# Performance work log

Hardware: AMD Instinct MI355X
Metric: run time of the kernel (lower is better)

The kernel has to match this reference:

```python
import jax, jax.numpy as jnp
import numpy as np
from jax import lax

B = 32768
IMG = 28
K = 3
OUT_HW = IMG - K + 1  # 26
FLAT = OUT_HW * OUT_HW  # 676
HID = 300
NCLS = 10


def setup_inputs() -> dict:
    key = jax.random.key(0)
    ks = jax.random.split(key, 8)
    x = jax.random.normal(ks[0], (B, IMG * IMG), dtype=jnp.float32)
    conv_w = jax.random.normal(ks[1], (K, K), dtype=jnp.float32) * 0.1
    # Linear params stored as (in, out) so forward is h @ W + b
    W1 = jax.random.normal(ks[2], (FLAT, HID), dtype=jnp.float32) * 0.04
    b1 = jnp.zeros((HID,), dtype=jnp.float32)
    W2 = jax.random.normal(ks[3], (HID, HID), dtype=jnp.float32) * 0.06
    b2 = jnp.zeros((HID,), dtype=jnp.float32)
    W3 = jax.random.normal(ks[4], (HID, NCLS), dtype=jnp.float32) * 0.06
    b3 = jnp.zeros((NCLS,), dtype=jnp.float32)
    return {"x": x, "conv_w": conv_w, "W1": W1, "b1": b1,
            "W2": W2, "b2": b2, "W3": W3, "b3": b3}


def reference(x, conv_w, W1, b1, W2, b2, W3, b3):
    b = x.shape[0]
    img = x.reshape(b, 1, IMG, IMG)  # NCHW
    # Valid cross-correlation with 3x3 kernel -> [B,1,26,26]
    y = lax.conv_general_dilated(
        img, conv_w[None, None, :, :], window_strides=(1, 1), padding="VALID",
        dimension_numbers=("NCHW", "OIHW", "NCHW"))
    h = y.reshape(b, FLAT)
    h = jax.nn.relu(h @ W1 + b1)
    h = jax.nn.relu(h @ W2 + b2)
    return h @ W3 + b3
```

## Files before the change

### kernel.cpp

```cpp
#include <hip/hip_runtime.h>


typedef __bf16 bf16_t;
typedef __bf16 bf16x8 __attribute__((ext_vector_type(8)));
typedef float  f32x4  __attribute__((ext_vector_type(4)));

#define MFMA16(a, b, c) __builtin_amdgcn_mfma_f32_16x16x32_bf16((a), (b), (c), 0, 0, 0)

#define W1F_ELEMS (25 * 20 * 64 * 8)
#define W2F_ELEMS (10 * 20 * 64 * 8)
#define W3F_ELEMS (10 * 1 * 64 * 8)

#define XSLOT 16384
#define XBASE 40960

__global__ void prep_weights(const float* __restrict__ conv_w,
                             const float* __restrict__ W1,
                             const float* __restrict__ W2,
                             const float* __restrict__ W3,
                             bf16_t* __restrict__ W1f,
                             bf16_t* __restrict__ W2f,
                             bf16_t* __restrict__ W3f) {
    int idx = blockIdx.x * 256 + threadIdx.x;
    if (idx < 800 * 320) {
        int k = idx / 320;
        int n = idx - k * 320;
        float v = 0.0f;
        if (k < 784 && n < 300) {
            int py = k / 28;
            int px = k - py * 28;
#pragma unroll
            for (int ky = 0; ky < 3; ++ky) {
                int oy = py - ky;
                if (oy < 0 || oy > 25) continue;
#pragma unroll
                for (int kx = 0; kx < 3; ++kx) {
                    int ox = px - kx;
                    if (ox < 0 || ox > 25) continue;
                    v += conv_w[ky * 3 + kx] * W1[(oy * 26 + ox) * 300 + n];
                }
            }
        }
        int kc = k >> 5, quad = (k >> 3) & 3, j = k & 7;
        int nt = n >> 4, nin = n & 15;
        W1f[(((kc * 20 + nt) * 64 + quad * 16 + nin) << 3) + j] = (bf16_t)v;
    } else if (idx < 800 * 320 + 320 * 320) {
        int i2 = idx - 800 * 320;
        int k = i2 / 320;
        int n = i2 - k * 320;
        float v = (k < 300 && n < 300) ? W2[k * 300 + n] : 0.0f;
        int kc = k >> 5, quad = (k >> 3) & 3, j = k & 7;
        int nt = n >> 4, nin = n & 15;
        W2f[(((kc * 20 + nt) * 64 + quad * 16 + nin) << 3) + j] = (bf16_t)v;
    } else if (idx < 800 * 320 + 320 * 320 + 320 * 16) {
        int i3 = idx - (800 * 320 + 320 * 320);
        int k = i3 / 16;
        int n = i3 - k * 16;
        float v = (k < 300 && n < 10) ? W3[k * 10 + n] : 0.0f;
        int kc = k >> 5, quad = (k >> 3) & 3, j = k & 7;
        W3f[(((kc * 64) + quad * 16 + n) << 3) + j] = (bf16_t)v;
    }
}

__device__ __forceinline__ void stage16(const void* g, void* l) {
    __builtin_amdgcn_global_load_lds(
        (const __attribute__((address_space(1))) void*)g,
        (__attribute__((address_space(3))) void*)l, 16, 0, 0);
}

__global__ __launch_bounds__(512, 4) void fused_mlp(
    const float* __restrict__ x, const float* __restrict__ b1,
    const float* __restrict__ b2, const float* __restrict__ b3,
    const bf16x8* __restrict__ W1f, const bf16x8* __restrict__ W2f,
    const bf16x8* __restrict__ W3f, float* __restrict__ out) {
    __shared__ __align__(16) unsigned char smem[XBASE + 2 * XSLOT];
    bf16x8* Bb   = (bf16x8*)smem;
    bf16x8* hbuf = (bf16x8*)smem;
    bf16_t* hb   = (bf16_t*)smem;

    const int tid = threadIdx.x;
    const int w   = tid >> 6;
    const int l   = tid & 63;
    const int q   = l >> 4;
    const int l15 = l & 15;
    const int r0  = blockIdx.x * 64;

    const bool t3    = (w < 4);
    const int  nt0   = t3 ? (w * 3) : (12 + (w - 4) * 2);
    const int  boff2 = t3 ? 128 : 64;

    f32x4 acc[4][3];
#pragma unroll
    for (int m = 0; m < 4; ++m)
#pragma unroll
        for (int j = 0; j < 3; ++j) acc[m][j] = (f32x4){0.f, 0.f, 0.f, 0.f};

#define STAGE_B(KC, BUF)                                                       \
    {                                                                          \
        const bf16x8* ws_ = W1f + (size_t)(KC)*1280 + l;                       \
        bf16x8* wd_ = Bb + (BUF)*1280;                                         \
        stage16(ws_ + w * 64, wd_ + w * 64);                                   \
        stage16(ws_ + (w + 8) * 64, wd_ + (w + 8) * 64);                       \
        if (w >= 4) stage16(ws_ + (w + 12) * 64, wd_ + (w + 12) * 64);         \
    }

#define STAGE_BAND(BAND)                                                       \
    {                                                                          \
        unsigned char* slot_ = smem + XBASE + ((BAND)&1) * XSLOT;              \
        if ((BAND) < 12) {                                                     \
            _Pragma("unroll")                                                  \
            for (int i_ = 0; i_ < 2; ++i_) {                                   \
                int row_ = w * 8 + i_ * 4 + (l >> 4);                          \
                int u_   = (l & 15) ^ (row_ & 7);                              \
                stage16(x + (size_t)(r0 + row_) * 784 + (BAND)*64 + u_ * 4,    \
                        slot_ + w * 2048 + i_ * 1024);                         \
            }                                                                  \
        } else {                                                               \
            int row_ = w * 8 + (l >> 3);                                       \
            int u_   = (l & 7) ^ (row_ & 7);                                   \
            const float* src_ = x + (size_t)(r0 + row_) * 784 +                \
                                ((u_ < 4) ? (768 + u_ * 4) : 0);               \
            stage16(src_, slot_ + w * 1024);                                   \
        }                                                                      \
    }

#define AFRAG(DST, SLOT, RS, KCL, MT)                                          \
    {                                                                          \
        int row_ = (MT)*16 + l15;                                              \
        int r7_  = row_ & 7;                                                   \
        float4 fa_ = *(const float4*)((SLOT) + row_ * (RS) +                   \
                     ((((KCL)*8 + q * 2 + 0) ^ r7_) << 4));                    \
        float4 fb_ = *(const float4*)((SLOT) + row_ * (RS) +                   \
                     ((((KCL)*8 + q * 2 + 1) ^ r7_) << 4));                    \
        bf16x8 t_;                                                             \
        t_[0] = (bf16_t)fa_.x; t_[1] = (bf16_t)fa_.y;                          \
        t_[2] = (bf16_t)fa_.z; t_[3] = (bf16_t)fa_.w;                          \
        t_[4] = (bf16_t)fb_.x; t_[5] = (bf16_t)fb_.y;                          \
        t_[6] = (bf16_t)fb_.z; t_[7] = (bf16_t)fb_.w;                          \
        DST = t_;                                                              \
    }

#define G1CHUNK(SLOT, RS, KCL, BUF)                                            \
    {                                                                          \
        bf16x8 a0, a1, a2, a3;                                                 \
        AFRAG(a0, SLOT, RS, KCL, 0) AFRAG(a1, SLOT, RS, KCL, 1)                \
        AFRAG(a2, SLOT, RS, KCL, 2) AFRAG(a3, SLOT, RS, KCL, 3)                \
        const bf16x8* bb_ = Bb + (BUF)*1280 + nt0 * 64 + l;                    \
        bf16x8 b0 = bb_[0], b1v = bb_[64], b2v = bb_[boff2];                   \
        acc[0][0] = MFMA16(a0, b0, acc[0][0]);                                 \
        acc[1][0] = MFMA16(a1, b0, acc[1][0]);                                 \
        acc[2][0] = MFMA16(a2, b0, acc[2][0]);                                 \
        acc[3][0] = MFMA16(a3, b0, acc[3][0]);                                 \
        acc[0][1] = MFMA16(a0, b1v, acc[0][1]);                                \
        acc[1][1] = MFMA16(a1, b1v, acc[1][1]);                                \
        acc[2][1] = MFMA16(a2, b1v, acc[2][1]);                                \
        acc[3][1] = MFMA16(a3, b1v, acc[3][1]);                                \
        if (t3) {                                                              \
            acc[0][2] = MFMA16(a0, b2v, acc[0][2]);                            \
            acc[1][2] = MFMA16(a1, b2v, acc[1][2]);                            \
            acc[2][2] = MFMA16(a2, b2v, acc[2][2]);                            \
            acc[3][2] = MFMA16(a3, b2v, acc[3][2]);                            \
        }                                                                      \
    }

#define VMW(N) asm volatile("s_waitcnt vmcnt(" #N ") lgkmcnt(0)" ::: "memory")
#define BARRIER()                         \
    __builtin_amdgcn_s_barrier();         \
    __builtin_amdgcn_sched_barrier(0)

    STAGE_B(0, 0)
    STAGE_BAND(0)
    VMW(0);
    BARRIER();

    for (int b = 0; b <= 10; ++b) {
        unsigned char* xs = smem + XBASE + (b & 1) * XSLOT;
        const int k0 = 2 * b;
        STAGE_B(k0 + 1, (k0 + 1) & 1)
        STAGE_BAND(b + 1)
        G1CHUNK(xs, 256, 0, k0 & 1)
        VMW(2);
        BARRIER();
        STAGE_B(k0 + 2, (k0 + 2) & 1)
        G1CHUNK(xs, 256, 1, (k0 + 1) & 1)
        VMW(0);
        BARRIER();
    }
    {
        unsigned char* xs = smem + XBASE + XSLOT;
        STAGE_B(23, 1)
        STAGE_BAND(12)
        G1CHUNK(xs, 256, 0, 0)
        VMW(1);
        BARRIER();
        STAGE_B(24, 0)
        G1CHUNK(xs, 256, 1, 1)
        VMW(0);
        BARRIER();
    }
    {
        unsigned char* xs = smem + XBASE;
        G1CHUNK(xs, 128, 0, 0)
        asm volatile("s_waitcnt lgkmcnt(0)" ::: "memory");
        BARRIER();
    }

#define HSTORE(J, BIAS)                                                        \
    {                                                                          \
        int n = (nt0 + (J)) * 16 + l15;                                        \
        float bias = (n < 300) ? (BIAS)[n] : 0.0f;                             \
        int kh = n >> 5, quad = (n >> 3) & 3, jj = n & 7;                      \
        _Pragma("unroll")                                                      \
        for (int mt = 0; mt < 4; ++mt)                                         \
            _Pragma("unroll")                                                  \
            for (int r = 0; r < 4; ++r) {                                      \
                float v = acc[mt][(J)][r] + bias;                              \
                v = v > 0.f ? v : 0.f;                                         \
                hb[(((kh * 4 + mt) * 64 + quad * 16 + q * 4 + r) << 3) + jj] = \
                    (bf16_t)v;                                                 \
            }                                                                  \
    }

    HSTORE(0, b1)
    HSTORE(1, b1)
    if (t3) HSTORE(2, b1)
    asm volatile("s_waitcnt lgkmcnt(0)" ::: "memory");
    BARRIER();

#pragma unroll
    for (int m = 0; m < 4; ++m)
#pragma unroll
        for (int j = 0; j < 3; ++j) acc[m][j] = (f32x4){0.f, 0.f, 0.f, 0.f};

    const bf16x8* bB2 = W2f + nt0 * 64 + l;

#define G2CHUNK(KC2)                                                           \
    {                                                                          \
        bf16x8 a0 = hbuf[((KC2)*4 + 0) * 64 + l];                              \
        bf16x8 a1 = hbuf[((KC2)*4 + 1) * 64 + l];                              \
        bf16x8 a2 = hbuf[((KC2)*4 + 2) * 64 + l];                              \
        bf16x8 a3 = hbuf[((KC2)*4 + 3) * 64 + l];                              \
        const bf16x8* bp = bB2 + (KC2)*1280;                                   \
        bf16x8 b0 = bp[0], b1v = bp[64], b2v = bp[boff2];                      \
        acc[0][0] = MFMA16(a0, b0, acc[0][0]);                                 \
        acc[1][0] = MFMA16(a1, b0, acc[1][0]);                                 \
        acc[2][0] = MFMA16(a2, b0, acc[2][0]);                                 \
        acc[3][0] = MFMA16(a3, b0, acc[3][0]);                                 \
        acc[0][1] = MFMA16(a0, b1v, acc[0][1]);                                \
        acc[1][1] = MFMA16(a1, b1v, acc[1][1]);                                \
        acc[2][1] = MFMA16(a2, b1v, acc[2][1]);                                \
        acc[3][1] = MFMA16(a3, b1v, acc[3][1]);                                \
        if (t3) {                                                              \
            acc[0][2] = MFMA16(a0, b2v, acc[0][2]);                            \
            acc[1][2] = MFMA16(a1, b2v, acc[1][2]);                            \
            acc[2][2] = MFMA16(a2, b2v, acc[2][2]);                            \
            acc[3][2] = MFMA16(a3, b2v, acc[3][2]);                            \
        }                                                                      \
    }

    G2CHUNK(0) G2CHUNK(1) G2CHUNK(2) G2CHUNK(3) G2CHUNK(4)
    G2CHUNK(5) G2CHUNK(6) G2CHUNK(7) G2CHUNK(8) G2CHUNK(9)

    asm volatile("s_waitcnt lgkmcnt(0)" ::: "memory");
    BARRIER();

    HSTORE(0, b2)
    HSTORE(1, b2)
    if (t3) HSTORE(2, b2)
    asm volatile("s_waitcnt lgkmcnt(0)" ::: "memory");
    BARRIER();

    if (w < 4) {
        f32x4 acc3 = (f32x4){0.f, 0.f, 0.f, 0.f};
#pragma unroll
        for (int kc3 = 0; kc3 < 10; ++kc3)
            acc3 = MFMA16(hbuf[(kc3 * 4 + w) * 64 + l], W3f[kc3 * 64 + l], acc3);
        if (l15 < 10) {
            float bias = b3[l15];
#pragma unroll
            for (int r = 0; r < 4; ++r)
                out[(size_t)(r0 + w * 16 + q * 4 + r) * 10 + l15] = acc3[r] + bias;
        }
    }
}

extern "C" void kernel_launch(void* const* d_in, const int* in_sizes, int n_in,
                              void* d_out, int out_size, void* d_ws, size_t ws_size,
                              hipStream_t stream) {
    const float* x      = (const float*)d_in[0];
    const float* conv_w = (const float*)d_in[1];
    const float* W1     = (const float*)d_in[2];
    const float* b1     = (const float*)d_in[3];
    const float* W2     = (const float*)d_in[4];
    const float* b2     = (const float*)d_in[5];
    const float* W3     = (const float*)d_in[6];
    const float* b3     = (const float*)d_in[7];
    float* out = (float*)d_out;

    char* ws = (char*)d_ws;
    bf16_t* W1f = (bf16_t*)(ws);
    bf16_t* W2f = (bf16_t*)(ws + (size_t)W1F_ELEMS * 2);
    bf16_t* W3f = (bf16_t*)(ws + (size_t)(W1F_ELEMS + W2F_ELEMS) * 2);
    if (ws_size < (size_t)(W1F_ELEMS + W2F_ELEMS + W3F_ELEMS) * 2) return;

    int prep_total = 800 * 320 + 320 * 320 + 320 * 16;
    prep_weights<<<(prep_total + 255) / 256, 256, 0, stream>>>(
        conv_w, W1, W2, W3, W1f, W2f, W3f);

    fused_mlp<<<32768 / 64, 512, 0, stream>>>(
        x, b1, b2, b3, (const bf16x8*)W1f, (const bf16x8*)W2f,
        (const bf16x8*)W3f, out);
}
```

Measured before the change: 181.2 us.

## Convert x bands to bf16 once in LDS via register prefetch

After: 188.7 us. 1.04x slower.

```diff
diff --git a/kernel.cpp b/kernel.cpp
--- a/kernel.cpp
+++ b/kernel.cpp
@@ -2,6 +2,7 @@
 
 
 typedef __bf16 bf16_t;
+typedef __bf16 bf16x4 __attribute__((ext_vector_type(4)));
 typedef __bf16 bf16x8 __attribute__((ext_vector_type(8)));
 typedef float  f32x4  __attribute__((ext_vector_type(4)));
 
@@ -83,12 +84,20 @@
     const int l   = tid & 63;
     const int q   = l >> 4;
     const int l15 = l & 15;
+    const int r7w = l15 & 7;
     const int r0  = blockIdx.x * 64;
 
     const bool t3    = (w < 4);
     const int  nt0   = t3 ? (w * 3) : (12 + (w - 4) * 2);
     const int  boff2 = t3 ? 128 : 64;
 
+    const int srow = tid >> 5;
+    const int sc4  = tid & 31;
+    const int sr7  = srow & 7;
+    const int trow = tid >> 3;
+    const int tc4  = tid & 7;
+
+    float4 pf[4];
     f32x4 acc[4][3];
 #pragma unroll
     for (int m = 0; m < 4; ++m)
@@ -104,47 +113,41 @@
         if (w >= 4) stage16(ws_ + (w + 12) * 64, wd_ + (w + 12) * 64);         \
     }
 
-#define STAGE_BAND(BAND)                                                       \
-    {                                                                          \
-        unsigned char* slot_ = smem + XBASE + ((BAND)&1) * XSLOT;              \
-        if ((BAND) < 12) {                                                     \
-            _Pragma("unroll")                                                  \
-            for (int i_ = 0; i_ < 2; ++i_) {                                   \
-                int row_ = w * 8 + i_ * 4 + (l >> 4);                          \
-                int u_   = (l & 15) ^ (row_ & 7);                              \
-                stage16(x + (size_t)(r0 + row_) * 784 + (BAND)*64 + u_ * 4,    \
-                        slot_ + w * 2048 + i_ * 1024);                         \
-            }                                                                  \
-        } else {                                                               \
-            int row_ = w * 8 + (l >> 3);                                       \
-            int u_   = (l & 7) ^ (row_ & 7);                                   \
-            const float* src_ = x + (size_t)(r0 + row_) * 784 +                \
-                                ((u_ < 4) ? (768 + u_ * 4) : 0);               \
-            stage16(src_, slot_ + w * 1024);                                   \
+#define LOADX(BAND, I)                                                         \
+    pf[I] = *(const float4*)(x + (size_t)(r0 + (I)*16 + srow) * 784 +          \
+                             (BAND)*128 + sc4 * 4);
+#define LOADX_B6()                                                             \
+    if (tc4 < 4)                                                               \
+        pf[0] = *(const float4*)(x + (size_t)(r0 + trow) * 784 + 768 + tc4 * 4);
+
+#define CVT_FULL(XW)                                                           \
+    {                                                                          \
+        const int pos_ = ((((sc4 >> 1) ^ sr7) << 4) + (sc4 & 1) * 8);          \
+        _Pragma("unroll")                                                      \
+        for (int i_ = 0; i_ < 4; ++i_) {                                       \
+            bf16x4 v_;                                                         \
+            v_[0] = (bf16_t)pf[i_].x; v_[1] = (bf16_t)pf[i_].y;                \
+            v_[2] = (bf16_t)pf[i_].z; v_[3] = (bf16_t)pf[i_].w;                \
+            *(bf16x4*)((XW) + (i_ * 16 + srow) * 256 + pos_) = v_;             \
         }                                                                      \
     }
-
-#define AFRAG(DST, SLOT, RS, KCL, MT)                                          \
-    {                                                                          \
-        int row_ = (MT)*16 + l15;                                              \
-        int r7_  = row_ & 7;                                                   \
-        float4 fa_ = *(const float4*)((SLOT) + row_ * (RS) +                   \
-                     ((((KCL)*8 + q * 2 + 0) ^ r7_) << 4));                    \
-        float4 fb_ = *(const float4*)((SLOT) + row_ * (RS) +                   \
-                     ((((KCL)*8 + q * 2 + 1) ^ r7_) << 4));                    \
-        bf16x8 t_;                                                             \
-        t_[0] = (bf16_t)fa_.x; t_[1] = (bf16_t)fa_.y;                          \
-        t_[2] = (bf16_t)fa_.z; t_[3] = (bf16_t)fa_.w;                          \
-        t_[4] = (bf16_t)fb_.x; t_[5] = (bf16_t)fb_.y;                          \
-        t_[6] = (bf16_t)fb_.z; t_[7] = (bf16_t)fb_.w;                          \
-        DST = t_;                                                              \
-    }
-
-#define G1CHUNK(SLOT, RS, KCL, BUF)                                            \
-    {                                                                          \
-        bf16x8 a0, a1, a2, a3;                                                 \
-        AFRAG(a0, SLOT, RS, KCL, 0) AFRAG(a1, SLOT, RS, KCL, 1)                \
-        AFRAG(a2, SLOT, RS, KCL, 2) AFRAG(a3, SLOT, RS, KCL, 3)                \
+#define CVT_B6(XW)                                                             \
+    if (tc4 < 4) {                                                             \
+        bf16x4 v_;                                                             \
+        v_[0] = (bf16_t)pf[0].x; v_[1] = (bf16_t)pf[0].y;                      \
+        v_[2] = (bf16_t)pf[0].z; v_[3] = (bf16_t)pf[0].w;                      \
+        *(bf16x4*)((XW) + trow * 256 +                                         \
+                   ((((tc4 >> 1) ^ (trow & 7)) << 4) + (tc4 & 1) * 8)) = v_;   \
+    }
+
+#define G1CHUNK16(SLOT, KCL, BUF)                                              \
+    {                                                                          \
+        const unsigned char* sp_ =                                             \
+            (SLOT) + l15 * 256 + (((((KCL)*4) + q) ^ r7w) << 4);               \
+        bf16x8 a0 = *(const bf16x8*)(sp_);                                     \
+        bf16x8 a1 = *(const bf16x8*)(sp_ + 4096);                              \
+        bf16x8 a2 = *(const bf16x8*)(sp_ + 8192);                              \
+        bf16x8 a3 = *(const bf16x8*)(sp_ + 12288);                             \
         const bf16x8* bb_ = Bb + (BUF)*1280 + nt0 * 64 + l;                    \
         bf16x8 b0 = bb_[0], b1v = bb_[64], b2v = bb_[boff2];                   \
         acc[0][0] = MFMA16(a0, b0, acc[0][0]);                                 \
@@ -169,38 +172,51 @@
     __builtin_amdgcn_sched_barrier(0)
 
     STAGE_B(0, 0)
-    STAGE_BAND(0)
-    VMW(0);
+    LOADX(0, 0) LOADX(0, 1) LOADX(0, 2) LOADX(0, 3)
+    { unsigned char* xw = smem + XBASE; CVT_FULL(xw) }
+    LOADX(1, 0) LOADX(1, 1) LOADX(1, 2) LOADX(1, 3)
+    VMW(4);
     BARRIER();
 
-    for (int b = 0; b <= 10; ++b) {
+    for (int b = 0; b <= 3; ++b) {
+        const int k0 = 4 * b;
         unsigned char* xs = smem + XBASE + (b & 1) * XSLOT;
-        const int k0 = 2 * b;
-        STAGE_B(k0 + 1, (k0 + 1) & 1)
-        STAGE_BAND(b + 1)
-        G1CHUNK(xs, 256, 0, k0 & 1)
-        VMW(2);
-        BARRIER();
-        STAGE_B(k0 + 2, (k0 + 2) & 1)
-        G1CHUNK(xs, 256, 1, (k0 + 1) & 1)
-        VMW(0);
-        BARRIER();
+        unsigned char* xw = smem + XBASE + ((b + 1) & 1) * XSLOT;
+        STAGE_B(k0 + 1, 1)
+        G1CHUNK16(xs, 0, 0)
+        CVT_FULL(xw)
+        VMW(0); BARRIER();
+        STAGE_B(k0 + 2, 0)
+        G1CHUNK16(xs, 1, 1)
+        VMW(0); BARRIER();
+        STAGE_B(k0 + 3, 1)
+        LOADX(b + 2, 0) LOADX(b + 2, 1)
+        G1CHUNK16(xs, 2, 0)
+        VMW(2); BARRIER();
+        STAGE_B(k0 + 4, 0)
+        LOADX(b + 2, 2) LOADX(b + 2, 3)
+        G1CHUNK16(xs, 3, 1)
+        VMW(2); BARRIER();
+    }
+    {
+        unsigned char* xs = smem + XBASE;
+        unsigned char* xw = smem + XBASE + XSLOT;
+        STAGE_B(17, 1) G1CHUNK16(xs, 0, 0) CVT_FULL(xw) VMW(0); BARRIER();
+        STAGE_B(18, 0) G1CHUNK16(xs, 1, 1) VMW(0); BARRIER();
+        STAGE_B(19, 1) G1CHUNK16(xs, 2, 0) VMW(0); BARRIER();
+        STAGE_B(20, 0) LOADX_B6() G1CHUNK16(xs, 3, 1) VMW(1); BARRIER();
     }
     {
         unsigned char* xs = smem + XBASE + XSLOT;
-        STAGE_B(23, 1)
-        STAGE_BAND(12)
-        G1CHUNK(xs, 256, 0, 0)
-        VMW(1);
-        BARRIER();
-        STAGE_B(24, 0)
-        G1CHUNK(xs, 256, 1, 1)
-        VMW(0);
-        BARRIER();
+        unsigned char* xw = smem + XBASE;
+        STAGE_B(21, 1) G1CHUNK16(xs, 0, 0) CVT_B6(xw) VMW(0); BARRIER();
+        STAGE_B(22, 0) G1CHUNK16(xs, 1, 1) VMW(0); BARRIER();
+        STAGE_B(23, 1) G1CHUNK16(xs, 2, 0) VMW(0); BARRIER();
+        STAGE_B(24, 0) G1CHUNK16(xs, 3, 1) VMW(0); BARRIER();
     }
     {
         unsigned char* xs = smem + XBASE;
-        G1CHUNK(xs, 128, 0, 0)
+        G1CHUNK16(xs, 0, 0)
         asm volatile("s_waitcnt lgkmcnt(0)" ::: "memory");
         BARRIER();
     }
```

## Halve workgroup to four waves, each computing five N-tiles

Applied to the files above, without the earlier changes.

Result: slower. 185.4 us (+2.3%).

```diff
diff --git a/kernel.cpp b/kernel.cpp
--- a/kernel.cpp
+++ b/kernel.cpp
@@ -68,7 +68,7 @@
         (__attribute__((address_space(3))) void*)l, 16, 0, 0);
 }
 
-__global__ __launch_bounds__(512, 4) void fused_mlp(
+__global__ __launch_bounds__(256, 2) void fused_mlp(
     const float* __restrict__ x, const float* __restrict__ b1,
     const float* __restrict__ b2, const float* __restrict__ b3,
     const bf16x8* __restrict__ W1f, const bf16x8* __restrict__ W2f,
@@ -85,23 +85,23 @@
     const int l15 = l & 15;
     const int r0  = blockIdx.x * 64;
 
-    const bool t3    = (w < 4);
-    const int  nt0   = t3 ? (w * 3) : (12 + (w - 4) * 2);
-    const int  boff2 = t3 ? 128 : 64;
-
-    f32x4 acc[4][3];
+    const int nt0 = w * 5;
+
+    f32x4 acc[4][5];
 #pragma unroll
     for (int m = 0; m < 4; ++m)
 #pragma unroll
-        for (int j = 0; j < 3; ++j) acc[m][j] = (f32x4){0.f, 0.f, 0.f, 0.f};
+        for (int j = 0; j < 5; ++j) acc[m][j] = (f32x4){0.f, 0.f, 0.f, 0.f};
 
 #define STAGE_B(KC, BUF)                                                       \
     {                                                                          \
         const bf16x8* ws_ = W1f + (size_t)(KC)*1280 + l;                       \
         bf16x8* wd_ = Bb + (BUF)*1280;                                         \
         stage16(ws_ + w * 64, wd_ + w * 64);                                   \
+        stage16(ws_ + (w + 4) * 64, wd_ + (w + 4) * 64);                       \
         stage16(ws_ + (w + 8) * 64, wd_ + (w + 8) * 64);                       \
-        if (w >= 4) stage16(ws_ + (w + 12) * 64, wd_ + (w + 12) * 64);         \
+        stage16(ws_ + (w + 12) * 64, wd_ + (w + 12) * 64);                     \
+        stage16(ws_ + (w + 16) * 64, wd_ + (w + 16) * 64);                     \
     }
 
 #define STAGE_BAND(BAND)                                                       \
@@ -109,18 +109,21 @@
         unsigned char* slot_ = smem + XBASE + ((BAND)&1) * XSLOT;              \
         if ((BAND) < 12) {                                                     \
             _Pragma("unroll")                                                  \
-            for (int i_ = 0; i_ < 2; ++i_) {                                   \
-                int row_ = w * 8 + i_ * 4 + (l >> 4);                          \
+            for (int i_ = 0; i_ < 4; ++i_) {                                   \
+                int row_ = w * 16 + i_ * 4 + (l >> 4);                         \
                 int u_   = (l & 15) ^ (row_ & 7);                              \
                 stage16(x + (size_t)(r0 + row_) * 784 + (BAND)*64 + u_ * 4,    \
-                        slot_ + w * 2048 + i_ * 1024);                         \
+                        slot_ + w * 4096 + i_ * 1024);                         \
             }                                                                  \
         } else {                                                               \
-            int row_ = w * 8 + (l >> 3);                                       \
-            int u_   = (l & 7) ^ (row_ & 7);                                   \
-            const float* src_ = x + (size_t)(r0 + row_) * 784 +                \
-                                ((u_ < 4) ? (768 + u_ * 4) : 0);               \
-            stage16(src_, slot_ + w * 1024);                                   \
+            _Pragma("unroll")                                                  \
+            for (int i_ = 0; i_ < 2; ++i_) {                                   \
+                int row_ = w * 16 + i_ * 8 + (l >> 3);                         \
+                int u_   = (l & 7) ^ (row_ & 7);                               \
+                const float* src_ = x + (size_t)(r0 + row_) * 784 +            \
+                                    ((u_ < 4) ? (768 + u_ * 4) : 0);           \
+                stage16(src_, slot_ + w * 2048 + i_ * 1024);                   \
+            }                                                                  \
         }                                                                      \
     }
 
@@ -146,7 +149,8 @@
         AFRAG(a0, SLOT, RS, KCL, 0) AFRAG(a1, SLOT, RS, KCL, 1)                \
         AFRAG(a2, SLOT, RS, KCL, 2) AFRAG(a3, SLOT, RS, KCL, 3)                \
         const bf16x8* bb_ = Bb + (BUF)*1280 + nt0 * 64 + l;                    \
-        bf16x8 b0 = bb_[0], b1v = bb_[64], b2v = bb_[boff2];                   \
+        bf16x8 b0 = bb_[0], b1v = bb_[64], b2v = bb_[128];                     \
+        bf16x8 b3v = bb_[192], b4v = bb_[256];                                 \
         acc[0][0] = MFMA16(a0, b0, acc[0][0]);                                 \
         acc[1][0] = MFMA16(a1, b0, acc[1][0]);                                 \
         acc[2][0] = MFMA16(a2, b0, acc[2][0]);                                 \
@@ -155,12 +159,18 @@
         acc[1][1] = MFMA16(a1, b1v, acc[1][1]);                                \
         acc[2][1] = MFMA16(a2, b1v, acc[2][1]);                                \
         acc[3][1] = MFMA16(a3, b1v, acc[3][1]);                                \
-        if (t3) {                                                              \
-            acc[0][2] = MFMA16(a0, b2v, acc[0][2]);                            \
-            acc[1][2] = MFMA16(a1, b2v, acc[1][2]);                            \
-            acc[2][2] = MFMA16(a2, b2v, acc[2][2]);                            \
-            acc[3][2] = MFMA16(a3, b2v, acc[3][2]);                            \
-        }                                                                      \
+        acc[0][2] = MFMA16(a0, b2v, acc[0][2]);                                \
+        acc[1][2] = MFMA16(a1, b2v, acc[1][2]);                                \
+        acc[2][2] = MFMA16(a2, b2v, acc[2][2]);                                \
+        acc[3][2] = MFMA16(a3, b2v, acc[3][2]);                                \
+        acc[0][3] = MFMA16(a0, b3v, acc[0][3]);                                \
+        acc[1][3] = MFMA16(a1, b3v, acc[1][3]);                                \
+        acc[2][3] = MFMA16(a2, b3v, acc[2][3]);                                \
+        acc[3][3] = MFMA16(a3, b3v, acc[3][3]);                                \
+        acc[0][4] = MFMA16(a0, b4v, acc[0][4]);                                \
+        acc[1][4] = MFMA16(a1, b4v, acc[1][4]);                                \
+        acc[2][4] = MFMA16(a2, b4v, acc[2][4]);                                \
+        acc[3][4] = MFMA16(a3, b4v, acc[3][4]);                                \
     }
 
 #define VMW(N) asm volatile("s_waitcnt vmcnt(" #N ") lgkmcnt(0)" ::: "memory")
@@ -179,7 +189,7 @@
         STAGE_B(k0 + 1, (k0 + 1) & 1)
         STAGE_BAND(b + 1)
         G1CHUNK(xs, 256, 0, k0 & 1)
-        VMW(2);
+        VMW(4);
         BARRIER();
         STAGE_B(k0 + 2, (k0 + 2) & 1)
         G1CHUNK(xs, 256, 1, (k0 + 1) & 1)
@@ -191,7 +201,7 @@
         STAGE_B(23, 1)
         STAGE_BAND(12)
         G1CHUNK(xs, 256, 0, 0)
-        VMW(1);
+        VMW(2);
         BARRIER();
         STAGE_B(24, 0)
         G1CHUNK(xs, 256, 1, 1)
@@ -221,16 +231,14 @@
             }                                                                  \
     }
 
-    HSTORE(0, b1)
-    HSTORE(1, b1)
-    if (t3) HSTORE(2, b1)
+    HSTORE(0, b1) HSTORE(1, b1) HSTORE(2, b1) HSTORE(3, b1) HSTORE(4, b1)
     asm volatile("s_waitcnt lgkmcnt(0)" ::: "memory");
     BARRIER();
 
 #pragma unroll
     for (int m = 0; m < 4; ++m)
 #pragma unroll
-        for (int j = 0; j < 3; ++j) acc[m][j] = (f32x4){0.f, 0.f, 0.f, 0.f};
+        for (int j = 0; j < 5; ++j) acc[m][j] = (f32x4){0.f, 0.f, 0.f, 0.f};
 
     const bf16x8* bB2 = W2f + nt0 * 64 + l;
 
@@ -241,7 +249,8 @@
         bf16x8 a2 = hbuf[((KC2)*4 + 2) * 64 + l];                              \
         bf16x8 a3 = hbuf[((KC2)*4 + 3) * 64 + l];                              \
         const bf16x8* bp = bB2 + (KC2)*1280;                                   \
-        bf16x8 b0 = bp[0], b1v = bp[64], b2v = bp[boff2];                      \
+        bf16x8 b0 = bp[0], b1v = bp[64], b2v = bp[128];                        \
+        bf16x8 b3v = bp[192], b4v = bp[256];                                   \
         acc[0][0] = MFMA16(a0, b0, acc[0][0]);                                 \
         acc[1][0] = MFMA16(a1, b0, acc[1][0]);                                 \
         acc[2][0] = MFMA16(a2, b0, acc[2][0]);                                 \
@@ -250,12 +259,18 @@
         acc[1][1] = MFMA16(a1, b1v, acc[1][1]);                                \
         acc[2][1] = MFMA16(a2, b1v, acc[2][1]);                                \
         acc[3][1] = MFMA16(a3, b1v, acc[3][1]);                                \
-        if (t3) {                                                              \
-            acc[0][2] = MFMA16(a0, b2v, acc[0][2]);                            \
-            acc[1][2] = MFMA16(a1, b2v, acc[1][2]);                            \
-            acc[2][2] = MFMA16(a2, b2v, acc[2][2]);                            \
-            acc[3][2] = MFMA16(a3, b2v, acc[3][2]);                            \
-        }                                                                      \
+        acc[0][2] = MFMA16(a0, b2v, acc[0][2]);                                \
+        acc[1][2] = MFMA16(a1, b2v, acc[1][2]);                                \
+        acc[2][2] = MFMA16(a2, b2v, acc[2][2]);                                \
+        acc[3][2] = MFMA16(a3, b2v, acc[3][2]);                                \
+        acc[0][3] = MFMA16(a0, b3v, acc[0][3]);                                \
+        acc[1][3] = MFMA16(a1, b3v, acc[1][3]);                                \
+        acc[2][3] = MFMA16(a2, b3v, acc[2][3]);                                \
+        acc[3][3] = MFMA16(a3, b3v, acc[3][3]);                                \
+        acc[0][4] = MFMA16(a0, b4v, acc[0][4]);                                \
+        acc[1][4] = MFMA16(a1, b4v, acc[1][4]);                                \
+        acc[2][4] = MFMA16(a2, b4v, acc[2][4]);                                \
+        acc[3][4] = MFMA16(a3, b4v, acc[3][4]);                                \
     }
 
     G2CHUNK(0) G2CHUNK(1) G2CHUNK(2) G2CHUNK(3) G2CHUNK(4)
@@ -264,13 +279,11 @@
     asm volatile("s_waitcnt lgkmcnt(0)" ::: "memory");
     BARRIER();
 
-    HSTORE(0, b2)
-    HSTORE(1, b2)
-    if (t3) HSTORE(2, b2)
+    HSTORE(0, b2) HSTORE(1, b2) HSTORE(2, b2) HSTORE(3, b2) HSTORE(4, b2)
     asm volatile("s_waitcnt lgkmcnt(0)" ::: "memory");
     BARRIER();
 
-    if (w < 4) {
+    {
         f32x4 acc3 = (f32x4){0.f, 0.f, 0.f, 0.f};
 #pragma unroll
         for (int kc3 = 0; kc3 < 10; ++kc3)
@@ -307,7 +320,7 @@
     prep_weights<<<(prep_total + 255) / 256, 256, 0, stream>>>(
         conv_w, W1, W2, W3, W1f, W2f, W3f);
 
-    fused_mlp<<<32768 / 64, 512, 0, stream>>>(
+    fused_mlp<<<32768 / 64, 256, 0, stream>>>(
         x, b1, b2, b3, (const bf16x8*)W1f, (const bf16x8*)W2f,
         (const bf16x8*)W3f, out);
 }
```

## Stage per-wave private W1 tiles and replace mid-chunk barriers with vmcnt waits

Applied to the files above, without the earlier changes.

New measurement: 186.0 us. 2.6% more time.

```diff
diff --git a/kernel.cpp b/kernel.cpp
--- a/kernel.cpp
+++ b/kernel.cpp
@@ -95,13 +95,13 @@
 #pragma unroll
         for (int j = 0; j < 3; ++j) acc[m][j] = (f32x4){0.f, 0.f, 0.f, 0.f};
 
-#define STAGE_B(KC, BUF)                                                       \
-    {                                                                          \
-        const bf16x8* ws_ = W1f + (size_t)(KC)*1280 + l;                       \
-        bf16x8* wd_ = Bb + (BUF)*1280;                                         \
-        stage16(ws_ + w * 64, wd_ + w * 64);                                   \
-        stage16(ws_ + (w + 8) * 64, wd_ + (w + 8) * 64);                       \
-        if (w >= 4) stage16(ws_ + (w + 12) * 64, wd_ + (w + 12) * 64);         \
+#define STAGE_BP(KC, BUF)                                                      \
+    {                                                                          \
+        const bf16x8* ws_ = W1f + (size_t)(KC)*1280 + nt0 * 64 + l;            \
+        bf16x8* wd_ = Bb + (BUF)*1280 + nt0 * 64;                              \
+        stage16(ws_, wd_);                                                     \
+        stage16(ws_ + 64, wd_ + 64);                                           \
+        if (t3) stage16(ws_ + 128, wd_ + 128);                                 \
     }
 
 #define STAGE_BAND(BAND)                                                       \
@@ -163,43 +163,51 @@
         }                                                                      \
     }
 
-#define VMW(N) asm volatile("s_waitcnt vmcnt(" #N ") lgkmcnt(0)" ::: "memory")
+#define VMW(N)   asm volatile("s_waitcnt vmcnt(" #N ")" ::: "memory")
+#define VMWLG(N) asm volatile("s_waitcnt vmcnt(" #N ") lgkmcnt(0)" ::: "memory")
+#define SCHED0() __builtin_amdgcn_sched_barrier(0)
 #define BARRIER()                         \
     __builtin_amdgcn_s_barrier();         \
-    __builtin_amdgcn_sched_barrier(0)
-
-    STAGE_B(0, 0)
+    SCHED0()
+
+    STAGE_BP(0, 0)
     STAGE_BAND(0)
-    VMW(0);
+    VMWLG(0);
     BARRIER();
 
     for (int b = 0; b <= 10; ++b) {
         unsigned char* xs = smem + XBASE + (b & 1) * XSLOT;
         const int k0 = 2 * b;
-        STAGE_B(k0 + 1, (k0 + 1) & 1)
+        STAGE_BP(k0 + 1, 1)
         STAGE_BAND(b + 1)
-        G1CHUNK(xs, 256, 0, k0 & 1)
-        VMW(2);
-        BARRIER();
-        STAGE_B(k0 + 2, (k0 + 2) & 1)
-        G1CHUNK(xs, 256, 1, (k0 + 1) & 1)
-        VMW(0);
+        if (t3) { VMW(5); } else { VMW(4); }
+        SCHED0();
+        G1CHUNK(xs, 256, 0, 0)
+        STAGE_BP(k0 + 2, 0)
+        if (t3) { VMW(5); } else { VMW(4); }
+        SCHED0();
+        G1CHUNK(xs, 256, 1, 1)
+        if (t3) { VMWLG(3); } else { VMWLG(2); }
         BARRIER();
     }
     {
         unsigned char* xs = smem + XBASE + XSLOT;
-        STAGE_B(23, 1)
+        STAGE_BP(23, 1)
         STAGE_BAND(12)
+        if (t3) { VMW(4); } else { VMW(3); }
+        SCHED0();
         G1CHUNK(xs, 256, 0, 0)
-        VMW(1);
-        BARRIER();
-        STAGE_B(24, 0)
+        STAGE_BP(24, 0)
+        if (t3) { VMW(4); } else { VMW(3); }
+        SCHED0();
         G1CHUNK(xs, 256, 1, 1)
-        VMW(0);
+        if (t3) { VMWLG(3); } else { VMWLG(2); }
         BARRIER();
     }
     {
         unsigned char* xs = smem + XBASE;
+        VMW(0);
+        SCHED0();
         G1CHUNK(xs, 128, 0, 0)
         asm volatile("s_waitcnt lgkmcnt(0)" ::: "memory");
         BARRIER();
```
